# Optimization experiments

Measured on AMD Instinct MI355X. Metric: run time of the kernel, lower is better.

Reference implementation:

```python
import jax, jax.numpy as jnp
import numpy as np

B, T, IN, H, NB, OUT = 256, 2048, 128, 256, 4, 8
BS = H // NB  # branch size = 64


def setup_inputs() -> dict:
    key = jax.random.key(0)
    ks = jax.random.split(key, 7)
    x = jax.random.normal(ks[0], (B, T, IN), dtype=jnp.float32)
    Wb = jax.random.normal(ks[1], (NB, IN, BS), dtype=jnp.float32) * (1.0 / np.sqrt(IN))
    bb = jax.random.normal(ks[2], (NB, BS), dtype=jnp.float32) * 0.05
    Wo = jax.random.normal(ks[3], (H, OUT), dtype=jnp.float32) * (1.0 / np.sqrt(H))
    bo = jax.random.normal(ks[4], (OUT,), dtype=jnp.float32) * 0.05
    # tau_m ~ U(0,4); tau_n branch i ~ U(-4+2i, -1+2i) per the torch init
    tau_m = jax.random.uniform(ks[5], (H,), dtype=jnp.float32, minval=0.0, maxval=4.0)
    lo = (-4.0 + 2.0 * jnp.arange(NB, dtype=jnp.float32))[:, None]
    tau_n = lo + 3.0 * jax.random.uniform(ks[6], (NB, BS), dtype=jnp.float32)
    return {"x": x, "Wb": Wb, "bb": bb, "Wo": Wo, "bo": bo,
            "tau_m": tau_m, "tau_n": tau_n}


def reference(x, Wb, bb, Wo, bo, tau_m, tau_n):
    Bsz = x.shape[0]
    # Batch all per-step branch projections into one einsum: [B,T,NB,BS] -> [B,T,H]
    # (branch i writes slice [i*BS:(i+1)*BS], which matches the reshape order)
    D = jnp.einsum('bti,nis->btns', x, Wb) + bb  # [B,T,NB,BS]
    D = D.reshape(Bsz, x.shape[1], -1)           # [B,T,H]

    beta = jax.nn.sigmoid(tau_n).reshape(-1)     # [H], per-branch smoothing
    alpha = jax.nn.sigmoid(tau_m)                # [H]

    def step(carry, d_t):
        c, m = carry
        c = beta * c + (1.0 - beta) * d_t        # dendritic current EMA
        m = alpha * m + (1.0 - alpha) * c        # membrane EMA
        o = jax.nn.sigmoid(m @ Wo + bo)          # [B,OUT]
        return (c, m), o

    init = (jnp.zeros((Bsz, D.shape[-1]), D.dtype),
            jnp.zeros((Bsz, D.shape[-1]), D.dtype))
    _, outs = jax.lax.scan(step, init, jnp.swapaxes(D, 0, 1))  # outs: [T,B,OUT]
    return jnp.swapaxes(outs, 0, 1)              # [B,T,OUT]
```

## Files before the change

### kernel.cpp

```cpp
#include <hip/hip_runtime.h>
#include <hip/hip_bf16.h>
#include <math.h>

#define DEVFN __device__ __forceinline__

typedef __attribute__((ext_vector_type(8))) __bf16 bf16x8;
typedef __attribute__((ext_vector_type(8))) short s16x8;
typedef __attribute__((ext_vector_type(4))) float f32x4;
typedef __attribute__((ext_vector_type(4))) unsigned int u32x4;

constexpr int Tt    = 2048;
constexpr int INt   = 128;
constexpr int Ht    = 256;
constexpr int OUTt  = 8;
constexpr int TT    = 64;
constexpr int NTILE = Tt / TT;

union Frag {
  s16x8 s;
  bf16x8 b;
  u32x4 u;
};

DEVFN unsigned short f2bf(float f) {
  unsigned int u = __builtin_bit_cast(unsigned int, f);
  u += 0x7fffu + ((u >> 16) & 1u);
  return (unsigned short)(u >> 16);
}

DEVFN unsigned int pack2(float lo, float hi) {
  return (unsigned int)f2bf(lo) | ((unsigned int)f2bf(hi) << 16);
}

__global__
__attribute__((amdgpu_flat_work_group_size(1024, 1024), amdgpu_waves_per_eu(4, 4)))
void sfnn_fused(
    const float* __restrict__ x, const float* __restrict__ Wb,
    const float* __restrict__ bb, const float* __restrict__ Wo,
    const float* __restrict__ bo, const float* __restrict__ tau_m,
    const float* __restrict__ tau_n, float* __restrict__ out)
{
  const int b    = blockIdx.x;
  const int tid  = threadIdx.x;
  const int lane = tid & 63;
  const int w    = tid >> 6;
  const int l16  = lane & 15;
  const int lhi  = lane >> 4;
  const int sid  = tid - 512;

  __shared__ __align__(16) unsigned char  Xb[2][TT * 256];
  __shared__ __align__(16) float          DfT[Ht * TT];
  __shared__ __align__(16) unsigned short Mb[TT * Ht];
  __shared__ __align__(16) unsigned short WoT[16 * Ht];

  const int   hch   = tid & 255;
  const float beta  = 1.f / (1.f + expf(-tau_n[hch]));
  const float alpha = 1.f / (1.f + expf(-tau_m[hch]));
  const float omb   = 1.f - beta;
  const float oma   = 1.f - alpha;
  const float bbh   = bb[hch];
  const float bo_l  = (l16 < OUTt) ? bo[l16] : 0.f;

  {
    const int j  = w;
    const int k0 = 4 * (tid & 63);
    float v0 = 0.f, v1 = 0.f, v2 = 0.f, v3 = 0.f;
    if (j < OUTt) {
      v0 = Wo[(k0 + 0) * OUTt + j]; v1 = Wo[(k0 + 1) * OUTt + j];
      v2 = Wo[(k0 + 2) * OUTt + j]; v3 = Wo[(k0 + 3) * OUTt + j];
    }
    unsigned long long pk = (unsigned long long)pack2(v0, v1) |
                            ((unsigned long long)pack2(v2, v3) << 32);
    *(unsigned long long*)(&WoT[j * 256 + (k0 ^ ((j & 7) << 3))]) = pk;
  }

  Frag Wf[4];
  {
    const int h = 16 * w + l16;
    const int n = h >> 6, s = h & 63;
    #pragma unroll
    for (int ks = 0; ks < 4; ++ks) {
      #pragma unroll
      for (int j = 0; j < 8; ++j) {
        const int i = 32 * ks + 8 * lhi + j;
        Wf[ks].s[j] = (short)f2bf(Wb[(n * 128 + i) * 64 + s]);
      }
    }
  }

  const float* xb   = x   + (size_t)b * Tt * INt;
  float*       outb = out + (size_t)b * Tt * OUTt;

  float c_s = 0.f, m_s = 0.f;
  f32x4 Q0, Q1, Q2, Q3;
  f32x4 dacc[4];

  #define BAR() do {                                                       \
    asm volatile("s_waitcnt lgkmcnt(0)" ::: "memory");                     \
    __builtin_amdgcn_s_barrier();                                          \
  } while (0)

  #define WAITVM0() do {                                                   \
    asm volatile("s_waitcnt vmcnt(0)" ::: "memory");                       \
    __builtin_amdgcn_sched_barrier(0);                                     \
  } while (0)

  #define ISSUE(TILE) do {                                                 \
    const float* _p = xb + (size_t)(TILE) * (TT * INt) + 4 * (size_t)sid;  \
    asm volatile("global_load_dwordx4 %0, %1, off" : "=&v"(Q0) : "v"(_p));         \
    asm volatile("global_load_dwordx4 %0, %1, off" : "=&v"(Q1) : "v"(_p + 2048));  \
    asm volatile("global_load_dwordx4 %0, %1, off" : "=&v"(Q2) : "v"(_p + 4096));  \
    asm volatile("global_load_dwordx4 %0, %1, off" : "=&v"(Q3) : "v"(_p + 6144));  \
  } while (0)

  #define STAGE(BUF) do {                                                  \
    WAITVM0();                                                             \
    const int kb = 8 * (sid & 31);                                         \
    const int tb = sid >> 5;                                               \
    f32x4 qq[4] = {Q0, Q1, Q2, Q3};                                        \
    _Pragma("unroll")                                                      \
    for (int q = 0; q < 4; ++q) {                                          \
      const int t = 16 * q + tb;                                           \
      unsigned long long pk = (unsigned long long)pack2(qq[q][0], qq[q][1]) |  \
            ((unsigned long long)pack2(qq[q][2], qq[q][3]) << 32);         \
      *(unsigned long long*)(&Xb[BUF][t * 256 + (kb ^ ((t & 7) << 4))]) = pk;  \
    }                                                                      \
  } while (0)

  #define GEMM(BUF) do {                                                   \
    _Pragma("unroll")                                                      \
    for (int tt = 0; tt < 4; ++tt) {                                       \
      dacc[tt] = f32x4{0.f, 0.f, 0.f, 0.f};                                \
      const int row = 16 * tt + l16;                                       \
      const int rs = row * 256, sw = (row & 7) << 4;                       \
      _Pragma("unroll")                                                    \
      for (int ks = 0; ks < 4; ++ks) {                                     \
        Frag a;                                                            \
        a.u = *(const u32x4*)(&Xb[BUF][rs + ((64 * ks + 16 * lhi) ^ sw)]); \
        dacc[tt] = __builtin_amdgcn_mfma_f32_16x16x32_bf16(                \
            a.b, Wf[ks].b, dacc[tt], 0, 0, 0);                             \
      }                                                                    \
    }                                                                      \
  } while (0)

  #define WRITEDF() do {                                                   \
    const int h = 16 * w + l16;                                            \
    const int hb = h * 64, dsw = (h & 7) << 2;                             \
    _Pragma("unroll")                                                      \
    for (int tt = 0; tt < 4; ++tt)                                         \
      *(f32x4*)(&DfT[hb + ((16 * tt + 4 * lhi) ^ dsw)]) = dacc[tt];        \
  } while (0)

  #define SCAN() do {                                                      \
    if (tid < 256) {                                                       \
      const int hb = tid * 64, dsw = (tid & 7) << 2;                       \
      _Pragma("unroll")                                                    \
      for (int g = 0; g < 4; ++g) {                                        \
        f32x4 dv[4];                                                       \
        _Pragma("unroll")                                                  \
        for (int q = 0; q < 4; ++q)                                        \
          dv[q] = *(const f32x4*)(&DfT[hb + ((16 * g + 4 * q) ^ dsw)]);    \
        _Pragma("unroll")                                                  \
        for (int q = 0; q < 4; ++q)                                        \
          _Pragma("unroll")                                                \
          for (int r = 0; r < 4; ++r) {                                    \
            const int t = 16 * g + 4 * q + r;                              \
            const float d = dv[q][r] + bbh;                                \
            c_s = fmaf(beta, c_s, omb * d);                                \
            m_s = fmaf(alpha, m_s, oma * c_s);                             \
            Mb[t * 256 + (tid ^ ((t & 7) << 3))] = f2bf(m_s);              \
          }                                                                \
      }                                                                    \
    }                                                                      \
  } while (0)

  #define PROJ(TI) do {                                                    \
    const int tp = w - 4;                                                  \
    const int trow = 16 * tp + l16;                                        \
    const int mrb = trow * 256, msw = (trow & 7) << 3;                     \
    const int wrb = l16 * 256,  wsw = (l16 & 7) << 3;                      \
    f32x4 p = f32x4{0.f, 0.f, 0.f, 0.f};                                   \
    _Pragma("unroll")                                                      \
    for (int ks = 0; ks < 8; ++ks) {                                       \
      const int k0 = 32 * ks + 8 * lhi;                                    \
      Frag ma, wo;                                                         \
      ma.u = *(const u32x4*)(&Mb[mrb + (k0 ^ msw)]);                       \
      wo.u = *(const u32x4*)(&WoT[wrb + (k0 ^ wsw)]);                      \
      p = __builtin_amdgcn_mfma_f32_16x16x32_bf16(ma.b, wo.b, p, 0, 0, 0); \
    }                                                                      \
    if (l16 < OUTt) {                                                      \
      _Pragma("unroll")                                                    \
      for (int r = 0; r < 4; ++r) {                                        \
        const int t = 16 * tp + 4 * lhi + r;                               \
        outb[(size_t)((TI) * TT + t) * OUTt + l16] =                       \
            1.f / (1.f + __expf(-(p[r] + bo_l)));                          \
      }                                                                    \
    }                                                                      \
  } while (0)

  if (w >= 8) {
    ISSUE(0); STAGE(0);
    ISSUE(1); STAGE(1);
  }
  BAR();
  GEMM(0);

  #define ITER(I, DOPROJ, DOGEMM, DOIS) do {                               \
    if (DOIS && w >= 8) ISSUE((I) + 2);                                    \
    WRITEDF();                                                             \
    if (DOPROJ && w >= 4 && w < 8) PROJ((I) - 1);                          \
    if (DOGEMM) GEMM(((I) + 1) & 1);                                       \
    BAR();                                                         \
    SCAN();                                                                \
    if (DOIS && w >= 8) STAGE((I) & 1);                                    \
    BAR();                                                         \
  } while (0)

  ITER(0, 0, 1, 1);
  for (int I = 1; I <= 29; ++I) ITER(I, 1, 1, 1);
  ITER(30, 1, 1, 0);
  ITER(31, 1, 0, 0);
  if (w >= 4 && w < 8) PROJ(31);

  #undef ISSUE
  #undef STAGE
  #undef GEMM
  #undef WRITEDF
  #undef SCAN
  #undef PROJ
  #undef ITER
  #undef BAR
  #undef WAITVM0
}

extern "C" void kernel_launch(void* const* d_in, const int* in_sizes, int n_in,
                              void* d_out, int out_size, void* d_ws, size_t ws_size,
                              hipStream_t stream) {
  const float* x     = (const float*)d_in[0];
  const float* Wb    = (const float*)d_in[1];
  const float* bb    = (const float*)d_in[2];
  const float* Wo    = (const float*)d_in[3];
  const float* bo    = (const float*)d_in[4];
  const float* tau_m = (const float*)d_in[5];
  const float* tau_n = (const float*)d_in[6];
  float* out = (float*)d_out;

  sfnn_fused<<<dim3(256), dim3(1024), 0, stream>>>(x, Wb, bb, Wo, bo, tau_m, tau_n, out);
}
```

Measured before the change: 106.4 us.

## Halve time tile, load x via global-to-LDS DMA with triple buffering

Shrinks the time tile from 64 to 32 steps, which doubles the number of barrier-separated iterations but shortens each scan phase. The x tile is now fetched with global_load_lds DMA into a three-deep raw fp32 LDS buffer, issued several tiles ahead, then converted to bf16 by four waves. Each GEMM wave now handles 32 hidden channels, so only eight waves run the GEMM, and the projection moves to waves 8-9. The aim is to hide global load latency behind the serial scan, at the cost of more LDS use and twice as many block barriers.

Result: slower. 179.0 us (+68.2%).

```diff
diff --git a/kernel.cpp b/kernel.cpp
--- a/kernel.cpp
+++ b/kernel.cpp
@@ -13,7 +13,7 @@
 constexpr int INt   = 128;
 constexpr int Ht    = 256;
 constexpr int OUTt  = 8;
-constexpr int TT    = 64;
+constexpr int TT    = 32;
 constexpr int NTILE = Tt / TT;
 
 union Frag {
@@ -32,8 +32,17 @@
   return (unsigned int)f2bf(lo) | ((unsigned int)f2bf(hi) << 16);
 }
 
+typedef __attribute__((address_space(3))) unsigned int lds_u32;
+typedef const __attribute__((address_space(1))) unsigned int glb_u32;
+
+DEVFN void dma16(const float* g, const float* l) {
+  __builtin_amdgcn_global_load_lds((glb_u32*)(uintptr_t)g,
+                                   (lds_u32*)(unsigned int)(uintptr_t)l,
+                                   16, 0, 0);
+}
+
 __global__
-__attribute__((amdgpu_flat_work_group_size(1024, 1024), amdgpu_waves_per_eu(4, 4)))
+__attribute__((amdgpu_flat_work_group_size(1024, 1024)))
 void sfnn_fused(
     const float* __restrict__ x, const float* __restrict__ Wb,
     const float* __restrict__ bb, const float* __restrict__ Wo,
@@ -46,8 +55,8 @@
   const int w    = tid >> 6;
   const int l16  = lane & 15;
   const int lhi  = lane >> 4;
-  const int sid  = tid - 512;
-
+
+  __shared__ __align__(16) float          Xraw[3][TT * INt];
   __shared__ __align__(16) unsigned char  Xb[2][TT * 256];
   __shared__ __align__(16) float          DfT[Ht * TT];
   __shared__ __align__(16) unsigned short Mb[TT * Ht];
@@ -74,16 +83,19 @@
     *(unsigned long long*)(&WoT[j * 256 + (k0 ^ ((j & 7) << 3))]) = pk;
   }
 
-  Frag Wf[4];
-  {
-    const int h = 16 * w + l16;
-    const int n = h >> 6, s = h & 63;
+  Frag Wf[2][4];
+  if (w < 8) {
     #pragma unroll
-    for (int ks = 0; ks < 4; ++ks) {
+    for (int nh = 0; nh < 2; ++nh) {
+      const int h = 32 * w + 16 * nh + l16;
+      const int n = h >> 6, s = h & 63;
       #pragma unroll
-      for (int j = 0; j < 8; ++j) {
-        const int i = 32 * ks + 8 * lhi + j;
-        Wf[ks].s[j] = (short)f2bf(Wb[(n * 128 + i) * 64 + s]);
+      for (int ks = 0; ks < 4; ++ks) {
+        #pragma unroll
+        for (int j = 0; j < 8; ++j) {
+          const int i = 32 * ks + 8 * lhi + j;
+          Wf[nh][ks].s[j] = (short)f2bf(Wb[(n * 128 + i) * 64 + s]);
+        }
       }
     }
   }
@@ -92,79 +104,93 @@
   float*       outb = out + (size_t)b * Tt * OUTt;
 
   float c_s = 0.f, m_s = 0.f;
-  f32x4 Q0, Q1, Q2, Q3;
-  f32x4 dacc[4];
+  f32x4 dacc[2][2];
 
   #define BAR() do {                                                       \
     asm volatile("s_waitcnt lgkmcnt(0)" ::: "memory");                     \
     __builtin_amdgcn_s_barrier();                                          \
   } while (0)
 
-  #define WAITVM0() do {                                                   \
-    asm volatile("s_waitcnt vmcnt(0)" ::: "memory");                       \
+  #define WAITVM(N) do {                                                   \
+    asm volatile("s_waitcnt vmcnt(" #N ")" ::: "memory");                  \
     __builtin_amdgcn_sched_barrier(0);                                     \
   } while (0)
 
-  #define ISSUE(TILE) do {                                                 \
-    const float* _p = xb + (size_t)(TILE) * (TT * INt) + 4 * (size_t)sid;  \
-    asm volatile("global_load_dwordx4 %0, %1, off" : "=&v"(Q0) : "v"(_p));         \
-    asm volatile("global_load_dwordx4 %0, %1, off" : "=&v"(Q1) : "v"(_p + 2048));  \
-    asm volatile("global_load_dwordx4 %0, %1, off" : "=&v"(Q2) : "v"(_p + 4096));  \
-    asm volatile("global_load_dwordx4 %0, %1, off" : "=&v"(Q3) : "v"(_p + 6144));  \
-  } while (0)
-
-  #define STAGE(BUF) do {                                                  \
-    WAITVM0();                                                             \
-    const int kb = 8 * (sid & 31);                                         \
-    const int tb = sid >> 5;                                               \
-    f32x4 qq[4] = {Q0, Q1, Q2, Q3};                                        \
+  #define ISSUE_DMA(TILE) do {                                             \
+    const int _bi = (TILE) % 3;                                            \
+    const float* _gs = xb + (size_t)(TILE) * (TT * INt);                   \
     _Pragma("unroll")                                                      \
     for (int q = 0; q < 4; ++q) {                                          \
-      const int t = 16 * q + tb;                                           \
-      unsigned long long pk = (unsigned long long)pack2(qq[q][0], qq[q][1]) |  \
-            ((unsigned long long)pack2(qq[q][2], qq[q][3]) << 32);         \
-      *(unsigned long long*)(&Xb[BUF][t * 256 + (kb ^ ((t & 7) << 4))]) = pk;  \
+      const int c = (w - 12) * 4 + q;                                      \
+      dma16(_gs + c * 256 + lane * 4, &Xraw[_bi][c * 256]);                \
+    }                                                                      \
+  } while (0)
+
+  #define CONVERT(TILE) do {                                               \
+    const int _bi = (TILE) % 3;                                            \
+    const int _bo = (TILE) & 1;                                            \
+    const int i8  = 8 * (lane & 31);              \
+    _Pragma("unroll")                                                      \
+    for (int q = 0; q < 4; ++q) {                                          \
+      const int c = (w - 12) * 4 + q;                                      \
+      const int t = 2 * c + (lane >> 5);                                   \
+      f32x4 v = *(const f32x4*)(&Xraw[_bi][256 * c + 4 * lane]);           \
+      unsigned long long pk = (unsigned long long)pack2(v[0], v[1]) |      \
+            ((unsigned long long)pack2(v[2], v[3]) << 32);                 \
+      *(unsigned long long*)(&Xb[_bo][t * 256 + (i8 ^ ((t & 7) << 4))]) = pk; \
     }                                                                      \
   } while (0)
 
   #define GEMM(BUF) do {                                                   \
     _Pragma("unroll")                                                      \
-    for (int tt = 0; tt < 4; ++tt) {                                       \
-      dacc[tt] = f32x4{0.f, 0.f, 0.f, 0.f};                                \
+    for (int tt = 0; tt < 2; ++tt) {                                       \
       const int row = 16 * tt + l16;                                       \
       const int rs = row * 256, sw = (row & 7) << 4;                       \
       _Pragma("unroll")                                                    \
       for (int ks = 0; ks < 4; ++ks) {                                     \
         Frag a;                                                            \
         a.u = *(const u32x4*)(&Xb[BUF][rs + ((64 * ks + 16 * lhi) ^ sw)]); \
-        dacc[tt] = __builtin_amdgcn_mfma_f32_16x16x32_bf16(                \
-            a.b, Wf[ks].b, dacc[tt], 0, 0, 0);                             \
-      }                                                                    \
-    }                                                                      \
+        _Pragma("unroll")                                                  \
+        for (int nh = 0; nh < 2; ++nh)                                     \
+          dacc[tt][nh] = __builtin_amdgcn_mfma_f32_16x16x32_bf16(          \
+              a.b, Wf[nh][ks].b, dacc[tt][nh], 0, 0, 0);                   \
+      }                                                                    \
+    }                                                                      \
+  } while (0)
+
+  #define GEMMZ(BUF) do {                                                  \
+    _Pragma("unroll")                                                      \
+    for (int tt = 0; tt < 2; ++tt)                                         \
+      _Pragma("unroll")                                                    \
+      for (int nh = 0; nh < 2; ++nh) dacc[tt][nh] = f32x4{0.f,0.f,0.f,0.f};\
+    GEMM(BUF);                                                             \
   } while (0)
 
   #define WRITEDF() do {                                                   \
-    const int h = 16 * w + l16;                                            \
-    const int hb = h * 64, dsw = (h & 7) << 2;                             \
-    _Pragma("unroll")                                                      \
-    for (int tt = 0; tt < 4; ++tt)                                         \
-      *(f32x4*)(&DfT[hb + ((16 * tt + 4 * lhi) ^ dsw)]) = dacc[tt];        \
+    _Pragma("unroll")                                                      \
+    for (int tt = 0; tt < 2; ++tt)                                         \
+      _Pragma("unroll")                                                    \
+      for (int nh = 0; nh < 2; ++nh) {                                     \
+        const int h = 32 * w + 16 * nh + l16;                              \
+        *(f32x4*)(&DfT[h * 32 + ((((4 * tt + lhi)) ^ (h & 7)) << 2)]) =    \
+            dacc[tt][nh];                                                  \
+      }                                                                    \
   } while (0)
 
   #define SCAN() do {                                                      \
     if (tid < 256) {                                                       \
-      const int hb = tid * 64, dsw = (tid & 7) << 2;                       \
-      _Pragma("unroll")                                                    \
-      for (int g = 0; g < 4; ++g) {                                        \
+      const int hb = tid * 32, hs = tid & 7;                               \
+      _Pragma("unroll")                                                    \
+      for (int gg = 0; gg < 2; ++gg) {                                     \
         f32x4 dv[4];                                                       \
         _Pragma("unroll")                                                  \
         for (int q = 0; q < 4; ++q)                                        \
-          dv[q] = *(const f32x4*)(&DfT[hb + ((16 * g + 4 * q) ^ dsw)]);    \
+          dv[q] = *(const f32x4*)(&DfT[hb + (((4 * gg + q) ^ hs) << 2)]);  \
         _Pragma("unroll")                                                  \
         for (int q = 0; q < 4; ++q)                                        \
           _Pragma("unroll")                                                \
           for (int r = 0; r < 4; ++r) {                                    \
-            const int t = 16 * g + 4 * q + r;                              \
+            const int t = 16 * gg + 4 * q + r;                             \
             const float d = dv[q][r] + bbh;                                \
             c_s = fmaf(beta, c_s, omb * d);                                \
             m_s = fmaf(alpha, m_s, oma * c_s);                             \
@@ -175,8 +201,8 @@
   } while (0)
 
   #define PROJ(TI) do {                                                    \
-    const int tp = w - 4;                                                  \
-    const int trow = 16 * tp + l16;                                        \
+    const int pw = w - 8;                                                  \
+    const int trow = 16 * pw + l16;                                        \
     const int mrb = trow * 256, msw = (trow & 7) << 3;                     \
     const int wrb = l16 * 256,  wsw = (l16 & 7) << 3;                      \
     f32x4 p = f32x4{0.f, 0.f, 0.f, 0.f};                                   \
@@ -191,46 +217,62 @@
     if (l16 < OUTt) {                                                      \
       _Pragma("unroll")                                                    \
       for (int r = 0; r < 4; ++r) {                                        \
-        const int t = 16 * tp + 4 * lhi + r;                               \
+        const int t = 16 * pw + 4 * lhi + r;                               \
         outb[(size_t)((TI) * TT + t) * OUTt + l16] =                       \
             1.f / (1.f + __expf(-(p[r] + bo_l)));                          \
       }                                                                    \
     }                                                                      \
   } while (0)
 
-  if (w >= 8) {
-    ISSUE(0); STAGE(0);
-    ISSUE(1); STAGE(1);
+  if (w >= 12) {
+    ISSUE_DMA(0); ISSUE_DMA(1); ISSUE_DMA(2);
+    WAITVM(8);
+    CONVERT(0);
+    asm volatile("s_waitcnt lgkmcnt(0)" ::: "memory");
+    ISSUE_DMA(3);
+    WAITVM(8);
+    CONVERT(1);
   }
   BAR();
-  GEMM(0);
-
-  #define ITER(I, DOPROJ, DOGEMM, DOIS) do {                               \
-    if (DOIS && w >= 8) ISSUE((I) + 2);                                    \
-    WRITEDF();                                                             \
-    if (DOPROJ && w >= 4 && w < 8) PROJ((I) - 1);                          \
-    if (DOGEMM) GEMM(((I) + 1) & 1);                                       \
+  if (w < 8) GEMMZ(0);
+
+  #define ITER(I, DOPROJ, DOGEMM, DOISS, DOCONV, WAITSTMT) do {            \
+    if (w < 8) {                                                           \
+      WRITEDF();                                                           \
+      if (DOGEMM) GEMMZ(((I) + 1) & 1);                                    \
+    } else if (DOPROJ && w < 10) {                                         \
+      PROJ((I) - 1);                                                       \
+    }                                                                      \
     BAR();                                                         \
     SCAN();                                                                \
-    if (DOIS && w >= 8) STAGE((I) & 1);                                    \
+    if (w >= 12) {                                                         \
+      if (DOISS) ISSUE_DMA((I) + 4);                                       \
+      WAITSTMT;                                                            \
+      if (DOCONV) CONVERT((I) + 2);                                        \
+    }                                                                      \
     BAR();                                                         \
   } while (0)
 
-  ITER(0, 0, 1, 1);
-  for (int I = 1; I <= 29; ++I) ITER(I, 1, 1, 1);
-  ITER(30, 1, 1, 0);
-  ITER(31, 1, 0, 0);
-  if (w >= 4 && w < 8) PROJ(31);
-
-  #undef ISSUE
-  #undef STAGE
+  ITER(0, 0, 1, 1, 1, WAITVM(8));
+  for (int I = 1; I <= 59; ++I) {
+    ITER(I, 1, 1, 1, 1, WAITVM(8));
+  }
+  ITER(60, 1, 1, 0, 1, WAITVM(4));
+  ITER(61, 1, 1, 0, 1, WAITVM(0));
+  ITER(62, 1, 1, 0, 0, (void)0);
+  ITER(63, 1, 0, 0, 0, (void)0);
+  if (w >= 8 && w < 10) PROJ(63);
+
+  #undef ISSUE_DMA
+  #undef CONVERT
   #undef GEMM
+  #undef GEMMZ
   #undef WRITEDF
   #undef SCAN
   #undef PROJ
   #undef ITER
   #undef BAR
-  #undef WAITVM0
+  #undef WAITVM
 }
 
 extern "C" void kernel_launch(void* const* d_in, const int* in_sizes, int n_in,
```

## Fuse branch GEMM and scan in-register with 32x32 MFMA, drop LDS D staging

Applied to the files above, without the earlier changes.

Eight waves now compute the branch projection with 32x32x16 MFMAs and run the EMA scan directly on the accumulator registers. Half-waves exchange the scan state via lane shuffles, which removes the DfT shared-memory round trip and leaves a single barrier per tile. The Mb buffer is double-buffered so two producer waves can run the output projection one tile behind while the others keep loading x, with loads issued two tiles ahead under partial vmcnt waits. The cost is that the serial scan now runs across eight waves with shuffles and predicated stores, and the waves-per-EU hint is dropped.

Result: slower. 140.5 us (+32.0%).

```diff
diff --git a/kernel.cpp b/kernel.cpp
--- a/kernel.cpp
+++ b/kernel.cpp
@@ -7,6 +7,7 @@
 typedef __attribute__((ext_vector_type(8))) __bf16 bf16x8;
 typedef __attribute__((ext_vector_type(8))) short s16x8;
 typedef __attribute__((ext_vector_type(4))) float f32x4;
+typedef __attribute__((ext_vector_type(16))) float f32x16;
 typedef __attribute__((ext_vector_type(4))) unsigned int u32x4;
 
 constexpr int Tt    = 2048;
@@ -14,7 +15,7 @@
 constexpr int Ht    = 256;
 constexpr int OUTt  = 8;
 constexpr int TT    = 64;
-constexpr int NTILE = Tt / TT;
+constexpr int NTILE = 32;
 
 union Frag {
   s16x8 s;
@@ -33,7 +34,7 @@
 }
 
 __global__
-__attribute__((amdgpu_flat_work_group_size(1024, 1024), amdgpu_waves_per_eu(4, 4)))
+__attribute__((amdgpu_flat_work_group_size(1024, 1024)))
 void sfnn_fused(
     const float* __restrict__ x, const float* __restrict__ Wb,
     const float* __restrict__ bb, const float* __restrict__ Wo,
@@ -46,20 +47,13 @@
   const int w    = tid >> 6;
   const int l16  = lane & 15;
   const int lhi  = lane >> 4;
+  const int l32  = lane & 31;
+  const int uh   = lane >> 5;
   const int sid  = tid - 512;
 
   __shared__ __align__(16) unsigned char  Xb[2][TT * 256];
-  __shared__ __align__(16) float          DfT[Ht * TT];
-  __shared__ __align__(16) unsigned short Mb[TT * Ht];
-  __shared__ __align__(16) unsigned short WoT[16 * Ht];
-
-  const int   hch   = tid & 255;
-  const float beta  = 1.f / (1.f + expf(-tau_n[hch]));
-  const float alpha = 1.f / (1.f + expf(-tau_m[hch]));
-  const float omb   = 1.f - beta;
-  const float oma   = 1.f - alpha;
-  const float bbh   = bb[hch];
-  const float bo_l  = (l16 < OUTt) ? bo[l16] : 0.f;
+  __shared__ __align__(16) unsigned short Mb[2][TT * 256];
+  __shared__ __align__(16) unsigned short WoT[16 * 256];
 
   {
     const int j  = w;
@@ -74,15 +68,22 @@
     *(unsigned long long*)(&WoT[j * 256 + (k0 ^ ((j & 7) << 3))]) = pk;
   }
 
-  Frag Wf[4];
-  {
-    const int h = 16 * w + l16;
-    const int n = h >> 6, s = h & 63;
+  const int   ch    = (32 * w + l32) & 255;
+  const float beta  = 1.f / (1.f + expf(-tau_n[ch]));
+  const float alpha = 1.f / (1.f + expf(-tau_m[ch]));
+  const float omb   = 1.f - beta;
+  const float oma   = 1.f - alpha;
+  const float bbh   = bb[ch];
+  const float bo_l  = (l16 < OUTt) ? bo[l16] : 0.f;
+
+  Frag Wf[8];
+  if (w < 8) {
+    const int n = ch >> 6, s = ch & 63;
     #pragma unroll
-    for (int ks = 0; ks < 4; ++ks) {
+    for (int ks = 0; ks < 8; ++ks) {
       #pragma unroll
       for (int j = 0; j < 8; ++j) {
-        const int i = 32 * ks + 8 * lhi + j;
+        const int i = 16 * ks + 8 * uh + j;
         Wf[ks].s[j] = (short)f2bf(Wb[(n * 128 + i) * 64 + s]);
       }
     }
@@ -91,146 +92,153 @@
   const float* xb   = x   + (size_t)b * Tt * INt;
   float*       outb = out + (size_t)b * Tt * OUTt;
 
-  float c_s = 0.f, m_s = 0.f;
-  f32x4 Q0, Q1, Q2, Q3;
-  f32x4 dacc[4];
+  float  c_s = 0.f, m_s = 0.f;
+  f32x16 dacc;
+  f32x4  QA0, QA1, QA2, QA3;
+  f32x4  QB0, QB1, QB2, QB3;
 
   #define BAR() do {                                                       \
     asm volatile("s_waitcnt lgkmcnt(0)" ::: "memory");                     \
     __builtin_amdgcn_s_barrier();                                          \
   } while (0)
 
-  #define WAITVM0() do {                                                   \
-    asm volatile("s_waitcnt vmcnt(0)" ::: "memory");                       \
+  #define WAITVM(N) do {                                                   \
+    asm volatile("s_waitcnt vmcnt(" #N ")" ::: "memory");                  \
     __builtin_amdgcn_sched_barrier(0);                                     \
   } while (0)
 
-  #define ISSUE(TILE) do {                                                 \
+  #define ISSUE(TILE, Q0, Q1, Q2, Q3) do {                                 \
     const float* _p = xb + (size_t)(TILE) * (TT * INt) + 4 * (size_t)sid;  \
-    asm volatile("global_load_dwordx4 %0, %1, off" : "=&v"(Q0) : "v"(_p));         \
-    asm volatile("global_load_dwordx4 %0, %1, off" : "=&v"(Q1) : "v"(_p + 2048));  \
-    asm volatile("global_load_dwordx4 %0, %1, off" : "=&v"(Q2) : "v"(_p + 4096));  \
-    asm volatile("global_load_dwordx4 %0, %1, off" : "=&v"(Q3) : "v"(_p + 6144));  \
-  } while (0)
-
-  #define STAGE(BUF) do {                                                  \
-    WAITVM0();                                                             \
+    asm volatile("global_load_dwordx4 %0, %1, off" : "=&v"(Q0) : "v"(_p));        \
+    asm volatile("global_load_dwordx4 %0, %1, off" : "=&v"(Q1) : "v"(_p + 2048)); \
+    asm volatile("global_load_dwordx4 %0, %1, off" : "=&v"(Q2) : "v"(_p + 4096)); \
+    asm volatile("global_load_dwordx4 %0, %1, off" : "=&v"(Q3) : "v"(_p + 6144)); \
+  } while (0)
+
+  #define STAGE(BUF, Q0, Q1, Q2, Q3) do {                                  \
     const int kb = 8 * (sid & 31);                                         \
-    const int tb = sid >> 5;                                               \
     f32x4 qq[4] = {Q0, Q1, Q2, Q3};                                        \
     _Pragma("unroll")                                                      \
     for (int q = 0; q < 4; ++q) {                                          \
-      const int t = 16 * q + tb;                                           \
+      const int t = 16 * q + (sid >> 5);                                   \
       unsigned long long pk = (unsigned long long)pack2(qq[q][0], qq[q][1]) |  \
             ((unsigned long long)pack2(qq[q][2], qq[q][3]) << 32);         \
       *(unsigned long long*)(&Xb[BUF][t * 256 + (kb ^ ((t & 7) << 4))]) = pk;  \
     }                                                                      \
   } while (0)
 
-  #define GEMM(BUF) do {                                                   \
-    _Pragma("unroll")                                                      \
-    for (int tt = 0; tt < 4; ++tt) {                                       \
-      dacc[tt] = f32x4{0.f, 0.f, 0.f, 0.f};                                \
-      const int row = 16 * tt + l16;                                       \
-      const int rs = row * 256, sw = (row & 7) << 4;                       \
-      _Pragma("unroll")                                                    \
-      for (int ks = 0; ks < 4; ++ks) {                                     \
-        Frag a;                                                            \
-        a.u = *(const u32x4*)(&Xb[BUF][rs + ((64 * ks + 16 * lhi) ^ sw)]); \
-        dacc[tt] = __builtin_amdgcn_mfma_f32_16x16x32_bf16(                \
-            a.b, Wf[ks].b, dacc[tt], 0, 0, 0);                             \
-      }                                                                    \
-    }                                                                      \
-  } while (0)
-
-  #define WRITEDF() do {                                                   \
-    const int h = 16 * w + l16;                                            \
-    const int hb = h * 64, dsw = (h & 7) << 2;                             \
-    _Pragma("unroll")                                                      \
-    for (int tt = 0; tt < 4; ++tt)                                         \
-      *(f32x4*)(&DfT[hb + ((16 * tt + 4 * lhi) ^ dsw)]) = dacc[tt];        \
-  } while (0)
-
-  #define SCAN() do {                                                      \
-    if (tid < 256) {                                                       \
-      const int hb = tid * 64, dsw = (tid & 7) << 2;                       \
-      _Pragma("unroll")                                                    \
-      for (int g = 0; g < 4; ++g) {                                        \
-        f32x4 dv[4];                                                       \
-        _Pragma("unroll")                                                  \
-        for (int q = 0; q < 4; ++q)                                        \
-          dv[q] = *(const f32x4*)(&DfT[hb + ((16 * g + 4 * q) ^ dsw)]);    \
-        _Pragma("unroll")                                                  \
-        for (int q = 0; q < 4; ++q)                                        \
-          _Pragma("unroll")                                                \
-          for (int r = 0; r < 4; ++r) {                                    \
-            const int t = 16 * g + 4 * q + r;                              \
-            const float d = dv[q][r] + bbh;                                \
-            c_s = fmaf(beta, c_s, omb * d);                                \
-            m_s = fmaf(alpha, m_s, oma * c_s);                             \
-            Mb[t * 256 + (tid ^ ((t & 7) << 3))] = f2bf(m_s);              \
-          }                                                                \
-      }                                                                    \
-    }                                                                      \
-  } while (0)
-
-  #define PROJ(TI) do {                                                    \
-    const int tp = w - 4;                                                  \
-    const int trow = 16 * tp + l16;                                        \
-    const int mrb = trow * 256, msw = (trow & 7) << 3;                     \
-    const int wrb = l16 * 256,  wsw = (l16 & 7) << 3;                      \
-    f32x4 p = f32x4{0.f, 0.f, 0.f, 0.f};                                   \
+  #define GEMMH(BUF, HH) do {                                              \
+    _Pragma("unroll")                                                      \
+    for (int ri = 0; ri < 16; ++ri) dacc[ri] = 0.f;                        \
+    const int row = 32 * (HH) + l32;                                       \
+    const int rs = row * 256, sw = (row & 7) << 4;                         \
     _Pragma("unroll")                                                      \
     for (int ks = 0; ks < 8; ++ks) {                                       \
-      const int k0 = 32 * ks + 8 * lhi;                                    \
-      Frag ma, wo;                                                         \
-      ma.u = *(const u32x4*)(&Mb[mrb + (k0 ^ msw)]);                       \
-      wo.u = *(const u32x4*)(&WoT[wrb + (k0 ^ wsw)]);                      \
-      p = __builtin_amdgcn_mfma_f32_16x16x32_bf16(ma.b, wo.b, p, 0, 0, 0); \
-    }                                                                      \
-    if (l16 < OUTt) {                                                      \
+      Frag a;                                                              \
+      a.u = *(const u32x4*)(&Xb[BUF][rs + ((32 * ks + 16 * uh) ^ sw)]);    \
+      dacc = __builtin_amdgcn_mfma_f32_32x32x16_bf16(a.b, Wf[ks].b, dacc, 0, 0, 0); \
+    }                                                                      \
+  } while (0)
+
+  #define SCANH(MBUF, HH) do {                                             \
+    _Pragma("unroll")                                                      \
+    for (int j = 0; j < 8; ++j) {                                          \
+      c_s = __shfl_xor(c_s, 32);                                           \
+      m_s = __shfl_xor(m_s, 32);                                           \
+      const bool act = (uh == ((j) & 1));                                  \
       _Pragma("unroll")                                                    \
       for (int r = 0; r < 4; ++r) {                                        \
-        const int t = 16 * tp + 4 * lhi + r;                               \
-        outb[(size_t)((TI) * TT + t) * OUTt + l16] =                       \
-            1.f / (1.f + __expf(-(p[r] + bo_l)));                          \
+        const float d = dacc[r + 4 * ((j) >> 1)] + bbh;                    \
+        c_s = fmaf(beta, c_s, omb * d);                                    \
+        m_s = fmaf(alpha, m_s, oma * c_s);                                 \
+        if (act) {                                                         \
+          const int t = 32 * (HH) + 4 * (j) + r;                           \
+          Mb[MBUF][t * 256 + (ch ^ ((t & 7) << 3))] = f2bf(m_s);           \
+        }                                                                  \
       }                                                                    \
     }                                                                      \
   } while (0)
 
+  #define PROJ(TI, MBUF) do {                                              \
+    _Pragma("unroll")                                                      \
+    for (int blk = 0; blk < 2; ++blk) {                                    \
+      const int pw2 = 2 * (w - 8) + blk;                                   \
+      const int trow = 16 * pw2 + l16;                                     \
+      const int mrb = trow * 256, msw = (trow & 7) << 3;                   \
+      const int wrb = l16 * 256,  wsw = (l16 & 7) << 3;                    \
+      f32x4 p = f32x4{0.f, 0.f, 0.f, 0.f};                                 \
+      _Pragma("unroll")                                                    \
+      for (int ks = 0; ks < 8; ++ks) {                                     \
+        const int k0 = 32 * ks + 8 * lhi;                                  \
+        Frag ma, wo;                                                       \
+        ma.u = *(const u32x4*)(&Mb[MBUF][mrb + (k0 ^ msw)]);               \
+        wo.u = *(const u32x4*)(&WoT[wrb + (k0 ^ wsw)]);                    \
+        p = __builtin_amdgcn_mfma_f32_16x16x32_bf16(ma.b, wo.b, p, 0, 0, 0); \
+      }                                                                    \
+      if (l16 < OUTt) {                                                    \
+        _Pragma("unroll")                                                  \
+        for (int r = 0; r < 4; ++r) {                                      \
+          const int t = 16 * pw2 + 4 * lhi + r;                            \
+          outb[(size_t)((TI) * TT + t) * OUTt + l16] =                     \
+              1.f / (1.f + __expf(-(p[r] + bo_l)));                        \
+        }                                                                  \
+      }                                                                    \
+    }                                                                      \
+  } while (0)
+
   if (w >= 8) {
-    ISSUE(0); STAGE(0);
-    ISSUE(1); STAGE(1);
+    ISSUE(0, QA0, QA1, QA2, QA3);
+    ISSUE(1, QB0, QB1, QB2, QB3);
+    WAITVM(4);
+    STAGE(0, QA0, QA1, QA2, QA3);
   }
   BAR();
-  GEMM(0);
-
-  #define ITER(I, DOPROJ, DOGEMM, DOIS) do {                               \
-    if (DOIS && w >= 8) ISSUE((I) + 2);                                    \
-    WRITEDF();                                                             \
-    if (DOPROJ && w >= 4 && w < 8) PROJ((I) - 1);                          \
-    if (DOGEMM) GEMM(((I) + 1) & 1);                                       \
-    BAR();                                                         \
-    SCAN();                                                                \
-    if (DOIS && w >= 8) STAGE((I) & 1);                                    \
-    BAR();                                                         \
-  } while (0)
-
-  ITER(0, 0, 1, 1);
-  for (int I = 1; I <= 29; ++I) ITER(I, 1, 1, 1);
-  ITER(30, 1, 1, 0);
-  ITER(31, 1, 0, 0);
-  if (w >= 4 && w < 8) PROJ(31);
+
+  #define ITER_EV(I, DOPROJ, DOISS, DOWAIT, WN, DOSTG) do {                \
+    if (w < 8) {                                                           \
+      GEMMH((I) & 1, 0); SCANH((I) & 1, 0);                                \
+      GEMMH((I) & 1, 1); SCANH((I) & 1, 1);                                \
+    } else {                                                               \
+      if (DOPROJ && w < 10) PROJ((I) - 1, ((I) - 1) & 1);                  \
+      if (DOISS) ISSUE((I) + 2, QA0, QA1, QA2, QA3);                       \
+      if (DOWAIT) WAITVM(WN);                                              \
+      if (DOSTG) STAGE(1, QB0, QB1, QB2, QB3);                             \
+    }                                                                      \
+    BAR();                                                                 \
+  } while (0)
+
+  #define ITER_OD(I, DOPROJ, DOISS, DOWAIT, WN, DOSTG) do {                \
+    if (w < 8) {                                                           \
+      GEMMH((I) & 1, 0); SCANH((I) & 1, 0);                                \
+      GEMMH((I) & 1, 1); SCANH((I) & 1, 1);                                \
+    } else {                                                               \
+      if (DOPROJ && w < 10) PROJ((I) - 1, ((I) - 1) & 1);                  \
+      if (DOISS) ISSUE((I) + 2, QB0, QB1, QB2, QB3);                       \
+      if (DOWAIT) WAITVM(WN);                                              \
+      if (DOSTG) STAGE(0, QA0, QA1, QA2, QA3);                             \
+    }                                                                      \
+    BAR();                                                                 \
+  } while (0)
+
+  ITER_EV(0, 0, 1, 1, 4, 1);
+  for (int ii = 0; ii < 14; ++ii) {
+    ITER_OD(2 * ii + 1, 1, 1, 1, 4, 1);
+    ITER_EV(2 * ii + 2, 1, 1, 1, 4, 1);
+  }
+  ITER_OD(29, 1, 1, 1, 4, 1);
+  ITER_EV(30, 1, 0, 1, 0, 1);
+  ITER_OD(31, 1, 0, 0, 0, 0);
+  if (w >= 8 && w < 10) PROJ(31, 1);
 
   #undef ISSUE
   #undef STAGE
-  #undef GEMM
-  #undef WRITEDF
-  #undef SCAN
+  #undef GEMMH
+  #undef SCANH
   #undef PROJ
-  #undef ITER
+  #undef ITER_EV
+  #undef ITER_OD
   #undef BAR
-  #undef WAITVM0
+  #undef WAITVM
 }
 
 extern "C" void kernel_launch(void* const* d_in, const int* in_sizes, int n_in,
```

## Scan two channels per thread in two waves and split x staging loads

Applied to the files above, without the earlier changes.

The recurrent scan now runs on two waves instead of four. Each thread advances two independent channel chains (ch and ch+128) and writes both as one packed 32-bit bf16 store into the membrane buffer. To match that interleaved layout, the Wo rows loaded into shared memory are permuted. The x tile loads are split into two batches of two dwordx4, with the second batch issued and waited on inside STAGE, which lowers register use but exposes more global-memory latency. The aim is more instruction-level parallelism and fewer LDS stores per step in the serial scan, at the cost of half as many scan threads.

Result: slower. 146.0 us (+37.2%).

```diff
diff --git a/kernel.cpp b/kernel.cpp
--- a/kernel.cpp
+++ b/kernel.cpp
@@ -14,7 +14,7 @@
 constexpr int Ht    = 256;
 constexpr int OUTt  = 8;
 constexpr int TT    = 64;
-constexpr int NTILE = Tt / TT;
+constexpr int NTILE = 32;
 
 union Frag {
   s16x8 s;
@@ -53,21 +53,15 @@
   __shared__ __align__(16) unsigned short Mb[TT * Ht];
   __shared__ __align__(16) unsigned short WoT[16 * Ht];
 
-  const int   hch   = tid & 255;
-  const float beta  = 1.f / (1.f + expf(-tau_n[hch]));
-  const float alpha = 1.f / (1.f + expf(-tau_m[hch]));
-  const float omb   = 1.f - beta;
-  const float oma   = 1.f - alpha;
-  const float bbh   = bb[hch];
-  const float bo_l  = (l16 < OUTt) ? bo[l16] : 0.f;
-
   {
     const int j  = w;
     const int k0 = 4 * (tid & 63);
     float v0 = 0.f, v1 = 0.f, v2 = 0.f, v3 = 0.f;
     if (j < OUTt) {
-      v0 = Wo[(k0 + 0) * OUTt + j]; v1 = Wo[(k0 + 1) * OUTt + j];
-      v2 = Wo[(k0 + 2) * OUTt + j]; v3 = Wo[(k0 + 3) * OUTt + j];
+      v0 = Wo[(((k0 + 0) & 1) * 128 + ((k0 + 0) >> 1)) * OUTt + j];
+      v1 = Wo[(((k0 + 1) & 1) * 128 + ((k0 + 1) >> 1)) * OUTt + j];
+      v2 = Wo[(((k0 + 2) & 1) * 128 + ((k0 + 2) >> 1)) * OUTt + j];
+      v3 = Wo[(((k0 + 3) & 1) * 128 + ((k0 + 3) >> 1)) * OUTt + j];
     }
     unsigned long long pk = (unsigned long long)pack2(v0, v1) |
                             ((unsigned long long)pack2(v2, v3) << 32);
@@ -88,42 +82,71 @@
     }
   }
 
+  float be0=0,om0=0,al0=0,oa0=0,bb0=0, be1=0,om1=0,al1=0,oa1=0,bb1=0;
+  if (w < 2) {
+    const int ch0 = 64 * w + lane;
+    be0 = 1.f/(1.f+expf(-tau_n[ch0]));       om0 = 1.f - be0;
+    al0 = 1.f/(1.f+expf(-tau_m[ch0]));       oa0 = 1.f - al0;
+    bb0 = bb[ch0];
+    be1 = 1.f/(1.f+expf(-tau_n[ch0+128]));   om1 = 1.f - be1;
+    al1 = 1.f/(1.f+expf(-tau_m[ch0+128]));   oa1 = 1.f - al1;
+    bb1 = bb[ch0+128];
+  }
+  const float bo_l = (l16 < OUTt) ? bo[l16] : 0.f;
+
   const float* xb   = x   + (size_t)b * Tt * INt;
   float*       outb = out + (size_t)b * Tt * OUTt;
 
-  float c_s = 0.f, m_s = 0.f;
-  f32x4 Q0, Q1, Q2, Q3;
+  float c0 = 0.f, m0 = 0.f, c1 = 0.f, m1 = 0.f;
   f32x4 dacc[4];
+  f32x4 Q0, Q1;
 
   #define BAR() do {                                                       \
     asm volatile("s_waitcnt lgkmcnt(0)" ::: "memory");                     \
     __builtin_amdgcn_s_barrier();                                          \
   } while (0)
 
-  #define WAITVM0() do {                                                   \
-    asm volatile("s_waitcnt vmcnt(0)" ::: "memory");                       \
+  #define WAITVM(N) do {                                                   \
+    asm volatile("s_waitcnt vmcnt(" #N ")" ::: "memory");                  \
     __builtin_amdgcn_sched_barrier(0);                                     \
   } while (0)
 
   #define ISSUE(TILE) do {                                                 \
     const float* _p = xb + (size_t)(TILE) * (TT * INt) + 4 * (size_t)sid;  \
-    asm volatile("global_load_dwordx4 %0, %1, off" : "=&v"(Q0) : "v"(_p));         \
-    asm volatile("global_load_dwordx4 %0, %1, off" : "=&v"(Q1) : "v"(_p + 2048));  \
-    asm volatile("global_load_dwordx4 %0, %1, off" : "=&v"(Q2) : "v"(_p + 4096));  \
-    asm volatile("global_load_dwordx4 %0, %1, off" : "=&v"(Q3) : "v"(_p + 6144));  \
-  } while (0)
-
-  #define STAGE(BUF) do {                                                  \
-    WAITVM0();                                                             \
+    asm volatile("global_load_dwordx4 %0, %1, off" : "=&v"(Q0) : "v"(_p));        \
+    asm volatile("global_load_dwordx4 %0, %1, off" : "=&v"(Q1) : "v"(_p + 2048)); \
+  } while (0)
+
+  #define STAGE(BUF, TILE) do {                                            \
     const int kb = 8 * (sid & 31);                                         \
-    const int tb = sid >> 5;                                               \
-    f32x4 qq[4] = {Q0, Q1, Q2, Q3};                                        \
-    _Pragma("unroll")                                                      \
-    for (int q = 0; q < 4; ++q) {                                          \
-      const int t = 16 * q + tb;                                           \
-      unsigned long long pk = (unsigned long long)pack2(qq[q][0], qq[q][1]) |  \
-            ((unsigned long long)pack2(qq[q][2], qq[q][3]) << 32);         \
-      *(unsigned long long*)(&Xb[BUF][t * 256 + (kb ^ ((t & 7) << 4))]) = pk;  \
+    WAITVM(0);                                                             \
+    {                                                                      \
+      const int t = (sid >> 5);                                            \
+      unsigned long long pk = (unsigned long long)pack2(Q0.x, Q0.y) |      \
+            ((unsigned long long)pack2(Q0.z, Q0.w) << 32);                 \
+      *(unsigned long long*)(&Xb[BUF][t * 256 + (kb ^ ((t & 7) << 4))]) = pk; \
+    }                                                                      \
+    {                                                                      \
+      const int t = 16 + (sid >> 5);                                       \
+      unsigned long long pk = (unsigned long long)pack2(Q1.x, Q1.y) |      \
+            ((unsigned long long)pack2(Q1.z, Q1.w) << 32);                 \
+      *(unsigned long long*)(&Xb[BUF][t * 256 + (kb ^ ((t & 7) << 4))]) = pk; \
+    }                                                                      \
+    const float* _p2 = xb + (size_t)(TILE) * (TT * INt) + 4 * (size_t)sid; \
+    asm volatile("global_load_dwordx4 %0, %1, off" : "=&v"(Q0) : "v"(_p2 + 4096)); \
+    asm volatile("global_load_dwordx4 %0, %1, off" : "=&v"(Q1) : "v"(_p2 + 6144)); \
+    WAITVM(0);                                                             \
+    {                                                                      \
+      const int t = 32 + (sid >> 5);                                       \
+      unsigned long long pk = (unsigned long long)pack2(Q0.x, Q0.y) |      \
+            ((unsigned long long)pack2(Q0.z, Q0.w) << 32);                 \
+      *(unsigned long long*)(&Xb[BUF][t * 256 + (kb ^ ((t & 7) << 4))]) = pk; \
+    }                                                                      \
+    {                                                                      \
+      const int t = 48 + (sid >> 5);                                       \
+      unsigned long long pk = (unsigned long long)pack2(Q1.x, Q1.y) |      \
+            ((unsigned long long)pack2(Q1.z, Q1.w) << 32);                 \
+      *(unsigned long long*)(&Xb[BUF][t * 256 + (kb ^ ((t & 7) << 4))]) = pk; \
     }                                                                      \
   } while (0)
 
@@ -152,24 +175,28 @@
   } while (0)
 
   #define SCAN() do {                                                      \
-    if (tid < 256) {                                                       \
-      const int hb = tid * 64, dsw = (tid & 7) << 2;                       \
+    if (w < 2) {                                                           \
+      const int ch0 = 64 * w + lane;                                       \
+      const int hb0 = ch0 * 64;                                            \
+      const int hb1 = hb0 + 128 * 64;                                      \
+      const int ds0 = (ch0 & 7) << 2;                \
+      const int p0  = 2 * ch0;                                             \
       _Pragma("unroll")                                                    \
-      for (int g = 0; g < 4; ++g) {                                        \
-        f32x4 dv[4];                                                       \
+      for (int q = 0; q < 16; ++q) {                                       \
+        f32x4 dv0 = *(const f32x4*)(&DfT[hb0 + ((4 * q) ^ ds0)]);          \
+        f32x4 dv1 = *(const f32x4*)(&DfT[hb1 + ((4 * q) ^ ds0)]);          \
         _Pragma("unroll")                                                  \
-        for (int q = 0; q < 4; ++q)                                        \
-          dv[q] = *(const f32x4*)(&DfT[hb + ((16 * g + 4 * q) ^ dsw)]);    \
-        _Pragma("unroll")                                                  \
-        for (int q = 0; q < 4; ++q)                                        \
-          _Pragma("unroll")                                                \
-          for (int r = 0; r < 4; ++r) {                                    \
-            const int t = 16 * g + 4 * q + r;                              \
-            const float d = dv[q][r] + bbh;                                \
-            c_s = fmaf(beta, c_s, omb * d);                                \
-            m_s = fmaf(alpha, m_s, oma * c_s);                             \
-            Mb[t * 256 + (tid ^ ((t & 7) << 3))] = f2bf(m_s);              \
-          }                                                                \
+        for (int r = 0; r < 4; ++r) {                                      \
+          const int t = 4 * q + r;                                         \
+          const float d0 = dv0[r] + bb0;                                   \
+          c0 = fmaf(be0, c0, om0 * d0);                                    \
+          m0 = fmaf(al0, m0, oa0 * c0);                                    \
+          const float d1 = dv1[r] + bb1;                                   \
+          c1 = fmaf(be1, c1, om1 * d1);                                    \
+          m1 = fmaf(al1, m1, oa1 * c1);                                    \
+          *(unsigned int*)(&Mb[t * 256 + (p0 ^ ((t & 7) << 3))]) =         \
+              pack2(m0, m1);                                               \
+        }                                                                  \
       }                                                                    \
     }                                                                      \
   } while (0)
@@ -199,20 +226,20 @@
   } while (0)
 
   if (w >= 8) {
-    ISSUE(0); STAGE(0);
-    ISSUE(1); STAGE(1);
+    ISSUE(0); STAGE(0, 0);
+    ISSUE(1); STAGE(1, 1);
   }
   BAR();
   GEMM(0);
 
   #define ITER(I, DOPROJ, DOGEMM, DOIS) do {                               \
-    if (DOIS && w >= 8) ISSUE((I) + 2);                                    \
+    if ((DOIS) && w >= 8) ISSUE((I) + 2);                                  \
     WRITEDF();                                                             \
-    if (DOPROJ && w >= 4 && w < 8) PROJ((I) - 1);                          \
+    if ((DOPROJ) && w >= 4 && w < 8) PROJ((I) - 1);                        \
     if (DOGEMM) GEMM(((I) + 1) & 1);                                       \
     BAR();                                                         \
     SCAN();                                                                \
-    if (DOIS && w >= 8) STAGE((I) & 1);                                    \
+    if ((DOIS) && w >= 8) STAGE((I) & 1, (I) + 2);                         \
     BAR();                                                         \
   } while (0)
 
@@ -230,7 +257,7 @@
   #undef PROJ
   #undef ITER
   #undef BAR
-  #undef WAITVM0
+  #undef WAITVM
 }
 
 extern "C" void kernel_launch(void* const* d_in, const int* in_sizes, int n_in,
```
